# Kernel tuning notes

Measured on AMD Instinct MI355X. Metric: run time of the kernel, lower is better.

The kernel has to match this reference:

```python
import jax, jax.numpy as jnp
import numpy as np

N = 50000   # nodes
E = 500000  # edges
NEG_SLOPE = 0.2


def _edge_softmax(e, dst, n):
    # softmax over edges grouped by destination node (DGL edge_softmax)
    m = jax.ops.segment_max(e, dst, num_segments=n)          # [N,H]
    ex = jnp.exp(e - m[dst])
    s = jax.ops.segment_sum(ex, dst, num_segments=n)
    return ex / s[dst]


def _gat(h, W, al, ar, b, src, dst, heads, d, Wres=None, act=True):
    # DGL GATConv (eval mode, no dropout)
    n = h.shape[0]
    feat = (h @ W).reshape(n, heads, d)                      # [N,H,D]
    el = jnp.sum(feat * al[None], axis=-1)                   # [N,H]
    er = jnp.sum(feat * ar[None], axis=-1)                   # [N,H]
    e = jax.nn.leaky_relu(el[src] + er[dst], NEG_SLOPE)      # [E,H]
    a = _edge_softmax(e, dst, n)                             # [E,H]
    rst = jax.ops.segment_sum(feat[src] * a[..., None], dst, num_segments=n)  # [N,H,D]
    if Wres is not None:
        res = (h @ Wres).reshape(n, heads, d)
    else:
        res = h.reshape(n, heads, d)                         # identity residual (in == heads*d)
    rst = rst + res + b.reshape(1, heads, d)
    if act:
        rst = jax.nn.elu(rst)
    return rst.reshape(n, heads * d)


def _bn(x, g, b, m, v):
    # BatchNorm1d in eval mode
    return (x - m) * g * jax.lax.rsqrt(v + 1e-5) + b


def setup_inputs() -> dict:
    key = jax.random.key(0)
    ks = jax.random.split(key, 40)
    rn = lambda i, s: jax.random.normal(ks[i], s, jnp.float32) * 0.1
    inp = dict(
        node_feats=jax.random.normal(ks[0], (N, 128), jnp.float32),
        edge_feats=jax.random.normal(ks[1], (E, 64), jnp.float32),
        src=jax.random.randint(ks[2], (E,), 0, N, jnp.int32),
        dst=jax.random.randint(ks[3], (E,), 0, N, jnp.int32),
        # GAT layer 0: 128 -> 8 heads x 16
        W0=rn(4, (128, 128)), al0=rn(5, (8, 16)), ar0=rn(6, (8, 16)), b0=rn(7, (128,)),
        g0=1.0 + rn(8, (128,)), bt0=rn(9, (128,)), m0=rn(10, (128,)),
        v0=1.0 + 0.1 * jax.random.uniform(ks[11], (128,), jnp.float32),
        # GAT layer 1: 128 -> 8 heads x 8 (residual projection)
        W1=rn(12, (128, 64)), al1=rn(13, (8, 8)), ar1=rn(14, (8, 8)), b1=rn(15, (64,)),
        Wres1=rn(16, (128, 64)),
        g1=1.0 + rn(17, (64,)), bt1=rn(18, (64,)), m1=rn(19, (64,)),
        v1=1.0 + 0.1 * jax.random.uniform(ks[20], (64,), jnp.float32),
        # GAT layer 2: 64 -> 1 head x 32 (residual projection, no activation)
        W2=rn(21, (64, 32)), al2=rn(22, (1, 32)), ar2=rn(23, (1, 32)), b2=rn(24, (32,)),
        Wres2=rn(25, (64, 32)),
        g2=1.0 + rn(26, (32,)), bt2=rn(27, (32,)), m2=rn(28, (32,)),
        v2=1.0 + 0.1 * jax.random.uniform(ks[29], (32,), jnp.float32),
        # edge projection 64 -> 128
        We=rn(30, (64, 128)), be=rn(31, (128,)),
        # edge classifier: 192 -> 32 -> 16 -> 2
        Wc1=rn(32, (192, 32)), bc1=rn(33, (32,)),
        Wc2=rn(34, (32, 16)), bc2=rn(35, (16,)),
        Wc3=rn(36, (16, 2)), bc3=rn(37, (2,)),
    )
    return inp


def reference(node_feats, edge_feats, src, dst,
              W0, al0, ar0, b0, g0, bt0, m0, v0,
              W1, al1, ar1, b1, Wres1, g1, bt1, m1, v1,
              W2, al2, ar2, b2, Wres2, g2, bt2, m2, v2,
              We, be, Wc1, bc1, Wc2, bc2, Wc3, bc3):
    h = _bn(_gat(node_feats, W0, al0, ar0, b0, src, dst, 8, 16), g0, bt0, m0, v0)
    h = _bn(_gat(h, W1, al1, ar1, b1, src, dst, 8, 8, Wres1), g1, bt1, m1, v1)
    h = _bn(_gat(h, W2, al2, ar2, b2, src, dst, 1, 32, Wres2, act=False), g2, bt2, m2, v2)
    ef = jax.nn.relu(edge_feats @ We + be)                   # [E,128]
    rep = jnp.concatenate([h[src], h[dst], ef], axis=1)      # [E,192]
    z = jax.nn.relu(rep @ Wc1 + bc1)
    z = jax.nn.relu(z @ Wc2 + bc2)
    return z @ Wc3 + bc3                                     # [E,2]
```

## Files before the change

### kernel.cpp

```cpp
#include <hip/hip_runtime.h>
#include <cfloat>
#include <math.h>

#define NEG_SLOPE 0.2f

typedef short short8 __attribute__((ext_vector_type(8)));
typedef float f32x4 __attribute__((ext_vector_type(4)));

__device__ __forceinline__ short f2bf(float x) {
    unsigned u = __float_as_uint(x);
    u += 0x7fffu + ((u >> 16) & 1u);
    return (short)(u >> 16);
}
__device__ __forceinline__ float bf2f(unsigned short s) {
    return __uint_as_float((unsigned)s << 16);
}

__device__ __forceinline__ void lds_fence() {
    __asm__ __volatile__("s_waitcnt lgkmcnt(0)" ::: "memory");
}


__global__ void count_deg_k(const int* __restrict__ dst, int* __restrict__ deg, int E) {
    int i = blockIdx.x * 256 + threadIdx.x;
    if (i < E) atomicAdd(&deg[dst[i]], 1);
}

__global__ void scanA_k(const int* __restrict__ deg, int* __restrict__ csum, int n) {
    int t = blockIdx.x * 256 + threadIdx.x;
    int ch = (n + 4095) >> 12;
    int beg = t * ch, end = min(beg + ch, n);
    int s = 0;
    for (int i = beg; i < end; ++i) s += deg[i];
    csum[t] = s;
}

__global__ void scanB_k(int* __restrict__ csum) {
    __shared__ int part[1024];
    int tid = threadIdx.x;
    int c[4];
    int s = 0;
#pragma unroll
    for (int i = 0; i < 4; ++i) { c[i] = csum[tid * 4 + i]; s += c[i]; }
    part[tid] = s;
    __syncthreads();
    for (int d = 1; d < 1024; d <<= 1) {
        int v = (tid >= d) ? part[tid - d] : 0;
        __syncthreads();
        part[tid] += v;
        __syncthreads();
    }
    int base = (tid > 0) ? part[tid - 1] : 0;
#pragma unroll
    for (int i = 0; i < 4; ++i) { csum[tid * 4 + i] = base; base += c[i]; }
}

__global__ void scanC_k(const int* __restrict__ deg, const int* __restrict__ csum,
                        int* __restrict__ off, int n, int E) {
    int t = blockIdx.x * 256 + threadIdx.x;
    int ch = (n + 4095) >> 12;
    int beg = t * ch, end = min(beg + ch, n);
    int run = csum[t];
    for (int i = beg; i < end; ++i) { off[i] = run; run += deg[i]; }
    if (t == 0) off[n] = E;
}

__global__ void scatter_k(const int* __restrict__ src, const int* __restrict__ dst,
                          const int* __restrict__ off, int* __restrict__ cur,
                          int* __restrict__ srcp, int E) {
    int i = blockIdx.x * 256 + threadIdx.x;
    if (i >= E) return;
    int d = dst[i];
    int p = off[d] + atomicAdd(&cur[d], 1);
    srcp[p] = src[i];
}


struct WSec { const float* src; short* dst; int K, OUT, base; };

__global__ void conv_w_k(const float* W0, const float* W1, const float* Wr1,
                         const float* W2, const float* Wr2, const float* Wc1,
                         const float* We, const float* Wc2,
                         short* W0T, short* W1T, short* Wr1T, short* W2T, short* Wr2T,
                         short* Wc1aT, short* Wc1bT, short* WeT, short* Wc1T, short* Wc2T) {
    int t = blockIdx.x * 256 + threadIdx.x;
    const float* src; short* dst; int K, OUT, base;
    if      (t < 16384) { src = W0;            dst = W0T;   K = 128; OUT = 128; base = 0; }
    else if (t < 24576) { src = W1;            dst = W1T;   K = 128; OUT = 64;  base = 16384; }
    else if (t < 32768) { src = Wr1;           dst = Wr1T;  K = 128; OUT = 64;  base = 24576; }
    else if (t < 34816) { src = W2;            dst = W2T;   K = 64;  OUT = 32;  base = 32768; }
    else if (t < 36864) { src = Wr2;           dst = Wr2T;  K = 64;  OUT = 32;  base = 34816; }
    else if (t < 37888) { src = Wc1;           dst = Wc1aT; K = 32;  OUT = 32;  base = 36864; }
    else if (t < 38912) { src = Wc1 + 1024;    dst = Wc1bT; K = 32;  OUT = 32;  base = 37888; }
    else if (t < 47104) { src = We;            dst = WeT;   K = 64;  OUT = 128; base = 38912; }
    else if (t < 51200) { src = Wc1 + 64 * 32; dst = Wc1T;  K = 128; OUT = 32;  base = 47104; }
    else if (t < 51712) { src = Wc2;           dst = Wc2T;  K = 32;  OUT = 16;  base = 51200; }
    else return;
    int local = t - base;
    int k = local / OUT, n = local % OUT;
    dst[n * K + k] = f2bf(src[k * OUT + n]);
}


template<int K, int NT1, int NT2, bool C1B16, bool AF32>
__global__ __launch_bounds__(256) void gemmM_k(const void* __restrict__ A,
                                               const short* __restrict__ B1T, void* __restrict__ C1,
                                               const short* __restrict__ B2T, float* __restrict__ C2,
                                               int N) {
    int w = threadIdx.x >> 6, lane = threadIdx.x & 63;
    int tile = blockIdx.x * 4 + w;
    int row0 = tile * 16;
    if (row0 >= N) return;
    int m = lane & 15, q = lane >> 4;
    int arow = row0 + m; if (arow >= N) arow = N - 1;

    constexpr int KT = K / 32;
    short8 Af[KT];
    if constexpr (AF32) {
        const float* Ap = (const float*)A + (size_t)arow * K;
#pragma unroll
        for (int kt = 0; kt < KT; ++kt) {
            float4 x = *(const float4*)&Ap[kt * 32 + q * 8];
            float4 y = *(const float4*)&Ap[kt * 32 + q * 8 + 4];
            short8 s;
            s[0] = f2bf(x.x); s[1] = f2bf(x.y); s[2] = f2bf(x.z); s[3] = f2bf(x.w);
            s[4] = f2bf(y.x); s[5] = f2bf(y.y); s[6] = f2bf(y.z); s[7] = f2bf(y.w);
            Af[kt] = s;
        }
    } else {
        const short* Ap = (const short*)A + (size_t)arow * K;
#pragma unroll
        for (int kt = 0; kt < KT; ++kt)
            Af[kt] = *(const short8*)&Ap[kt * 32 + q * 8];
    }

#pragma unroll
    for (int nt = 0; nt < NT1; ++nt) {
        f32x4 acc = {0.f, 0.f, 0.f, 0.f};
#pragma unroll
        for (int kt = 0; kt < KT; ++kt) {
            short8 b = *(const short8*)&B1T[(size_t)(nt * 16 + m) * K + kt * 32 + q * 8];
            acc = __builtin_amdgcn_mfma_f32_16x16x32_bf16(Af[kt], b, acc, 0, 0, 0);
        }
#pragma unroll
        for (int r = 0; r < 4; ++r) {
            int row = row0 + q * 4 + r;
            if (row < N) {
                if constexpr (C1B16)
                    ((short*)C1)[(size_t)row * (NT1 * 16) + nt * 16 + m] = f2bf(acc[r]);
                else
                    ((float*)C1)[(size_t)row * (NT1 * 16) + nt * 16 + m] = acc[r];
            }
        }
    }
    if constexpr (NT2 > 0) {
#pragma unroll
        for (int nt = 0; nt < NT2; ++nt) {
            f32x4 acc = {0.f, 0.f, 0.f, 0.f};
#pragma unroll
            for (int kt = 0; kt < KT; ++kt) {
                short8 b = *(const short8*)&B2T[(size_t)(nt * 16 + m) * K + kt * 32 + q * 8];
                acc = __builtin_amdgcn_mfma_f32_16x16x32_bf16(Af[kt], b, acc, 0, 0, 0);
            }
#pragma unroll
            for (int r = 0; r < 4; ++r) {
                int row = row0 + q * 4 + r;
                if (row < N)
                    C2[(size_t)row * (NT2 * 16) + nt * 16 + m] = acc[r];
            }
        }
    }
}


template<int H, int D>
__global__ void elr_k(const short* __restrict__ featb, const float* __restrict__ al,
                      const float* __restrict__ ar, float* __restrict__ el,
                      float* __restrict__ er, int n) {
    int i = blockIdx.x * 256 + threadIdx.x;
    if (i >= n * H) return;
    int h = i % H;
    const short* f = featb + (size_t)(i / H) * (H * D) + h * D;
    float sl = 0.f, sr = 0.f;
#pragma unroll
    for (int d = 0; d < D; ++d) {
        float v = bf2f((unsigned short)f[d]);
        sl = fmaf(v, al[h * D + d], sl);
        sr = fmaf(v, ar[h * D + d], sr);
    }
    el[i] = sl; er[i] = sr;
}


template<int H, int D, bool ACT>
__global__ __launch_bounds__(256) void gat_node2_k(
    const int* __restrict__ off, const int* __restrict__ srcp,
    const float* __restrict__ el, const float* __restrict__ er,
    const short* __restrict__ featb,
    const float* __restrict__ res, const float* __restrict__ bias,
    const float* __restrict__ bg, const float* __restrict__ bb,
    const float* __restrict__ bm, const float* __restrict__ bv,
    short* __restrict__ houtb, int N) {
    constexpr int HD = H * D;
    constexpr bool PAIR = (HD > 64);
    constexpr int CH = 64 / H;
    int wv_ = threadIdx.x >> 6;
    int lane = threadIdx.x & 63;
    int n = blockIdx.x * 4 + wv_;
    if (n >= N) return;
    int beg = off[n], end = off[n + 1];

    int hh = lane % H;
    int cc = lane / H;
    float ern = er[(size_t)n * H + hh];

    int k0 = PAIR ? 2 * lane : lane;
    int h0 = k0 / D; if (h0 > H - 1) h0 = H - 1;

    float acc0 = 0.f, acc1 = 0.f, svp = 0.f;

    for (int i0 = beg; i0 < end; i0 += CH) {
        int iw = i0 + cc;
        float wv = 0.f;
        int sidx = 0;
        if (iw < end) {
            sidx = srcp[iw];
            float x = el[(size_t)sidx * H + hh] + ern;
            x = x > 0.f ? x : NEG_SLOPE * x;
            wv = __expf(x);
        }
        svp += wv;
        int lim = min(end - i0, CH);
        for (int r = 0; r < lim; ++r) {
            int sl = r * H + h0;
            float w0 = __shfl(wv, sl, 64);
            int s    = __shfl(sidx, sl, 64);
            if constexpr (PAIR) {
                ushort2 uv = *(const ushort2*)&featb[(size_t)s * HD + k0];
                acc0 = fmaf(w0, bf2f(uv.x), acc0);
                acc1 = fmaf(w0, bf2f(uv.y), acc1);
            } else {
                if (lane < HD)
                    acc0 = fmaf(w0, bf2f((unsigned short)featb[(size_t)s * HD + k0]), acc0);
            }
        }
    }
#pragma unroll
    for (int mm = H; mm < 64; mm <<= 1) svp += __shfl_xor(svp, mm, 64);
    bool has_edges = end > beg;
    float inv0 = has_edges ? 1.f / __shfl(svp, h0, 64) : 0.f;

    if constexpr (PAIR) {
        float2 rs = *(const float2*)&res[(size_t)n * HD + k0];
        float2 bi = *(const float2*)&bias[k0];
        float2 gm = *(const float2*)&bm[k0];
        float2 gv = *(const float2*)&bv[k0];
        float2 gg = *(const float2*)&bg[k0];
        float2 gb = *(const float2*)&bb[k0];
        float x0 = acc0 * inv0 + rs.x + bi.x;
        float x1 = acc1 * inv0 + rs.y + bi.y;
        if (ACT) { x0 = x0 > 0.f ? x0 : expm1f(x0); x1 = x1 > 0.f ? x1 : expm1f(x1); }
        float o0 = (x0 - gm.x) * (gg.x * rsqrtf(gv.x + 1e-5f)) + gb.x;
        float o1 = (x1 - gm.y) * (gg.y * rsqrtf(gv.y + 1e-5f)) + gb.y;
        ushort2 hb;
        hb.x = (unsigned short)f2bf(o0);
        hb.y = (unsigned short)f2bf(o1);
        *(ushort2*)&houtb[(size_t)n * HD + k0] = hb;
    } else {
        if (lane < HD) {
            int k = k0;
            float x = acc0 * inv0 + res[(size_t)n * HD + k] + bias[k];
            if (ACT) x = x > 0.f ? x : expm1f(x);
            float o = (x - bm[k]) * (bg[k] * rsqrtf(bv[k] + 1e-5f)) + bb[k];
            houtb[(size_t)n * HD + k] = f2bf(o);
        }
    }
}


__global__ __launch_bounds__(256) void edge_cls_k(
    const float* __restrict__ u1, const float* __restrict__ u2,
    const float* __restrict__ edf,
    const int* __restrict__ src, const int* __restrict__ dst,
    const short* __restrict__ WeTg, const float* __restrict__ be,
    const short* __restrict__ Wc1Tg, const float* __restrict__ bc1,
    const short* __restrict__ Wc2Tg, const float* __restrict__ bc2,
    const float* __restrict__ Wc3, const float* __restrict__ bc3,
    float* __restrict__ out, int E) {
    __shared__ short efA[4][16 * 136];
    __shared__ short z1A[4][16 * 40];
    __shared__ float z2A[4][16 * 20];

    int t = threadIdx.x;
    int w = t >> 6, lane = t & 63;
    int m = lane & 15, q = lane >> 4;
    short* efW = efA[w];
    short* z1W = z1A[w];
    float* z2W = z2A[w];

    int tiles = (E + 15) >> 4;
    int gw = blockIdx.x * 4 + w;
    int W  = gridDim.x * 4;

    float beh[8];
#pragma unroll
    for (int nt = 0; nt < 8; ++nt) beh[nt] = be[nt * 16 + m];
    float bc1h0 = bc1[m], bc1h1 = bc1[16 + m];
    float bc2h = bc2[m];
    float bc30 = bc3[0], bc31 = bc3[1];

    auto ldrow = [&](int tl, float4& a, float4& b, float4& c, float4& d) {
        int em = tl * 16 + m;
        const float* rp = edf + (size_t)(em < E ? em : E - 1) * 64;
        a = *(const float4*)(rp + q * 8);
        b = *(const float4*)(rp + q * 8 + 4);
        c = *(const float4*)(rp + 32 + q * 8);
        d = *(const float4*)(rp + 32 + q * 8 + 4);
    };

    int tile = gw;
    float4 p0 = {0,0,0,0}, p1 = p0, p2 = p0, p3 = p0;
    if (tile < tiles) ldrow(tile, p0, p1, p2, p3);

    for (; tile < tiles; tile += W) {
        float4 c0 = p0, c1 = p1, c2 = p2, c3 = p3;
        int tn = tile + W;
        if (tn < tiles) ldrow(tn, p0, p1, p2, p3);

        int e0w = tile * 16;

        float u1g[2][4], u2g[2][4];
#pragma unroll
        for (int r = 0; r < 4; ++r) {
            int e = e0w + q * 4 + r;
            int ec = e < E ? e : E - 1;
            int s = src[ec], d = dst[ec];
            u1g[0][r] = u1[(size_t)s * 32 + m];
            u1g[1][r] = u1[(size_t)s * 32 + 16 + m];
            u2g[0][r] = u2[(size_t)d * 32 + m];
            u2g[1][r] = u2[(size_t)d * 32 + 16 + m];
        }

        short8 A0, A1;
        A0[0] = f2bf(c0.x); A0[1] = f2bf(c0.y); A0[2] = f2bf(c0.z); A0[3] = f2bf(c0.w);
        A0[4] = f2bf(c1.x); A0[5] = f2bf(c1.y); A0[6] = f2bf(c1.z); A0[7] = f2bf(c1.w);
        A1[0] = f2bf(c2.x); A1[1] = f2bf(c2.y); A1[2] = f2bf(c2.z); A1[3] = f2bf(c2.w);
        A1[4] = f2bf(c3.x); A1[5] = f2bf(c3.y); A1[6] = f2bf(c3.z); A1[7] = f2bf(c3.w);

#pragma unroll
        for (int nt = 0; nt < 8; ++nt) {
            int col = nt * 16 + m;
            float bias = beh[nt];
            f32x4 acc = {bias, bias, bias, bias};
            short8 b0 = *(const short8*)&WeTg[col * 64 + q * 8];
            short8 b1 = *(const short8*)&WeTg[col * 64 + 32 + q * 8];
            acc = __builtin_amdgcn_mfma_f32_16x16x32_bf16(A0, b0, acc, 0, 0, 0);
            acc = __builtin_amdgcn_mfma_f32_16x16x32_bf16(A1, b1, acc, 0, 0, 0);
#pragma unroll
            for (int r = 0; r < 4; ++r)
                efW[(q * 4 + r) * 136 + col] = f2bf(fmaxf(acc[r], 0.f));
        }
        lds_fence();

        short8 Az[4];
#pragma unroll
        for (int kt = 0; kt < 4; ++kt)
            Az[kt] = *(const short8*)&efW[m * 136 + kt * 32 + q * 8];
#pragma unroll
        for (int nt = 0; nt < 2; ++nt) {
            int col = nt * 16 + m;
            float bias = nt ? bc1h1 : bc1h0;
            f32x4 acc = {bias, bias, bias, bias};
#pragma unroll
            for (int kt = 0; kt < 4; ++kt) {
                short8 b = *(const short8*)&Wc1Tg[col * 128 + kt * 32 + q * 8];
                acc = __builtin_amdgcn_mfma_f32_16x16x32_bf16(Az[kt], b, acc, 0, 0, 0);
            }
#pragma unroll
            for (int r = 0; r < 4; ++r) {
                float z = acc[r] + u1g[nt][r] + u2g[nt][r];
                z1W[(q * 4 + r) * 40 + col] = f2bf(fmaxf(z, 0.f));
            }
        }
        lds_fence();

        {
            short8 Az1 = *(const short8*)&z1W[m * 40 + q * 8];
            short8 Bz  = *(const short8*)&Wc2Tg[m * 32 + q * 8];
            f32x4 acc = {bc2h, bc2h, bc2h, bc2h};
            acc = __builtin_amdgcn_mfma_f32_16x16x32_bf16(Az1, Bz, acc, 0, 0, 0);
#pragma unroll
            for (int r = 0; r < 4; ++r)
                z2W[(q * 4 + r) * 20 + m] = fmaxf(acc[r], 0.f);
        }
        lds_fence();

        if (lane < 16) {
            int e = lane;
            int eg = e0w + e;
            if (eg < E) {
                float a0 = bc30, a1 = bc31;
#pragma unroll
                for (int k = 0; k < 16; ++k) {
                    float z = z2W[e * 20 + k];
                    a0 = fmaf(z, Wc3[k * 2], a0);
                    a1 = fmaf(z, Wc3[k * 2 + 1], a1);
                }
                float2 o = {a0, a1};
                *(float2*)&out[(size_t)eg * 2] = o;
            }
        }
        lds_fence();
    }
}


extern "C" void kernel_launch(void* const* d_in, const int* in_sizes, int n_in,
                              void* d_out, int out_size, void* d_ws, size_t ws_size,
                              hipStream_t stream) {
    const float* node_feats = (const float*)d_in[0];
    const float* edge_feats = (const float*)d_in[1];
    const int*   src  = (const int*)d_in[2];
    const int*   dst  = (const int*)d_in[3];
    const float* W0   = (const float*)d_in[4];
    const float* al0  = (const float*)d_in[5];
    const float* ar0  = (const float*)d_in[6];
    const float* b0   = (const float*)d_in[7];
    const float* g0   = (const float*)d_in[8];
    const float* bt0  = (const float*)d_in[9];
    const float* m0   = (const float*)d_in[10];
    const float* v0   = (const float*)d_in[11];
    const float* W1   = (const float*)d_in[12];
    const float* al1  = (const float*)d_in[13];
    const float* ar1  = (const float*)d_in[14];
    const float* b1   = (const float*)d_in[15];
    const float* Wr1  = (const float*)d_in[16];
    const float* g1   = (const float*)d_in[17];
    const float* bt1  = (const float*)d_in[18];
    const float* m1   = (const float*)d_in[19];
    const float* v1   = (const float*)d_in[20];
    const float* W2   = (const float*)d_in[21];
    const float* al2  = (const float*)d_in[22];
    const float* ar2  = (const float*)d_in[23];
    const float* b2   = (const float*)d_in[24];
    const float* Wr2  = (const float*)d_in[25];
    const float* g2   = (const float*)d_in[26];
    const float* bt2  = (const float*)d_in[27];
    const float* v2m  = (const float*)d_in[28];
    const float* v2v  = (const float*)d_in[29];
    const float* We   = (const float*)d_in[30];
    const float* be   = (const float*)d_in[31];
    const float* Wc1  = (const float*)d_in[32];
    const float* bc1  = (const float*)d_in[33];
    const float* Wc2  = (const float*)d_in[34];
    const float* bc2  = (const float*)d_in[35];
    const float* Wc3  = (const float*)d_in[36];
    const float* bc3  = (const float*)d_in[37];
    float* out = (float*)d_out;

    const int N = in_sizes[0] / 128;
    const int E = in_sizes[2];

    char* p = (char*)d_ws;
    auto alloc = [&](size_t bytes) -> void* {
        void* r = (void*)p;
        p += (bytes + 255) & ~(size_t)255;
        return r;
    };
    int*   deg   = (int*)alloc((size_t)N * 4);
    int*   cur   = (int*)alloc((size_t)N * 4);
    int*   off   = (int*)alloc((size_t)(N + 1) * 4);
    int*   srcp  = (int*)alloc((size_t)E * 4);
    int*   csum  = (int*)alloc(4096 * 4);
    short* featb = (short*)alloc((size_t)N * 128 * 2);
    short* h1b   = (short*)alloc((size_t)N * 128 * 2);
    short* h2b   = (short*)alloc((size_t)N * 64 * 2);
    short* h3b   = (short*)alloc((size_t)N * 32 * 2);
    float* resf  = (float*)alloc((size_t)N * 64 * 4);
    float* u1    = (float*)alloc((size_t)N * 32 * 4);
    float* u2    = (float*)alloc((size_t)N * 32 * 4);
    float* el    = (float*)alloc((size_t)N * 8 * 4);
    float* er    = (float*)alloc((size_t)N * 8 * 4);
    short* W0T   = (short*)alloc(128 * 128 * 2);
    short* W1T   = (short*)alloc(64 * 128 * 2);
    short* Wr1T  = (short*)alloc(64 * 128 * 2);
    short* W2T   = (short*)alloc(32 * 64 * 2);
    short* Wr2T  = (short*)alloc(32 * 64 * 2);
    short* Wc1aT = (short*)alloc(32 * 32 * 2);
    short* Wc1bT = (short*)alloc(32 * 32 * 2);
    short* WeTg  = (short*)alloc(128 * 64 * 2);
    short* Wc1Tg = (short*)alloc(32 * 128 * 2);
    short* Wc2Tg = (short*)alloc(16 * 32 * 2);

    hipMemsetAsync(deg, 0, (size_t)N * 4, stream);
    hipMemsetAsync(cur, 0, (size_t)N * 4, stream);

    int eb = (E + 255) / 256;
    count_deg_k<<<eb, 256, 0, stream>>>(dst, deg, E);
    scanA_k<<<16, 256, 0, stream>>>(deg, csum, N);
    scanB_k<<<1, 1024, 0, stream>>>(csum);
    scanC_k<<<16, 256, 0, stream>>>(deg, csum, off, N, E);
    scatter_k<<<eb, 256, 0, stream>>>(src, dst, off, cur, srcp, E);
    conv_w_k<<<202, 256, 0, stream>>>(W0, W1, Wr1, W2, Wr2, Wc1, We, Wc2,
                                      W0T, W1T, Wr1T, W2T, Wr2T,
                                      Wc1aT, Wc1bT, WeTg, Wc1Tg, Wc2Tg);

    int nb4 = (N + 3) / 4;
    int gtb = ((N + 15) / 16 + 3) / 4;

    gemmM_k<128, 8, 0, true, true><<<gtb, 256, 0, stream>>>(node_feats, W0T, featb, nullptr, nullptr, N);
    elr_k<8, 16><<<(N * 8 + 255) / 256, 256, 0, stream>>>(featb, al0, ar0, el, er, N);
    gat_node2_k<8, 16, true><<<nb4, 256, 0, stream>>>(off, srcp, el, er, featb, node_feats,
                                                      b0, g0, bt0, m0, v0, h1b, N);
    gemmM_k<128, 4, 4, true, false><<<gtb, 256, 0, stream>>>(h1b, W1T, featb, Wr1T, resf, N);
    elr_k<8, 8><<<(N * 8 + 255) / 256, 256, 0, stream>>>(featb, al1, ar1, el, er, N);
    gat_node2_k<8, 8, true><<<nb4, 256, 0, stream>>>(off, srcp, el, er, featb, resf,
                                                     b1, g1, bt1, m1, v1, h2b, N);
    gemmM_k<64, 2, 2, true, false><<<gtb, 256, 0, stream>>>(h2b, W2T, featb, Wr2T, resf, N);
    elr_k<1, 32><<<(N + 255) / 256, 256, 0, stream>>>(featb, al2, ar2, el, er, N);
    gat_node2_k<1, 32, false><<<nb4, 256, 0, stream>>>(off, srcp, el, er, featb, resf,
                                                       b2, g2, bt2, v2m, v2v, h3b, N);
    gemmM_k<32, 2, 2, false, false><<<gtb, 256, 0, stream>>>(h3b, Wc1aT, u1, Wc1bT, u2, N);
    edge_cls_k<<<1024, 256, 0, stream>>>(u1, u2, edge_feats, src, dst,
                                         WeTg, be, Wc1Tg, bc1,
                                         Wc2Tg, bc2, Wc3, bc3, out, E);
}
```

Before: 577.6 us.

## Batch neighbor gathers in GAT aggregation, simplify CSR scatter, shuffle-reduce edge classifier

The GAT aggregation kernel now shuffles up to eight edge weights and indices at once and issues all the feature-row loads before the FMAs, so several independent gathers are in flight per wavefront. CSR construction records each edge's atomic rank during degree counting, which removes the second atomic pass and its memset. The edge classifier computes the final 16->2 layer with cross-lane shuffle reductions instead of an LDS round trip, and drops a shared buffer. It also gains a launch-bounds occupancy hint and a grid sized to the tile count. Costs are more registers per thread and an extra E-sized rank array.

```diff
diff --git a/kernel.cpp b/kernel.cpp
--- a/kernel.cpp
+++ b/kernel.cpp
@@ -5,6 +5,7 @@
 #define NEG_SLOPE 0.2f
 
 typedef short short8 __attribute__((ext_vector_type(8)));
+typedef short short4v __attribute__((ext_vector_type(4)));
 typedef float f32x4 __attribute__((ext_vector_type(4)));
 
 __device__ __forceinline__ short f2bf(float x) {
@@ -21,9 +22,10 @@
 }
 
 
-__global__ void count_deg_k(const int* __restrict__ dst, int* __restrict__ deg, int E) {
+__global__ void count_deg_k(const int* __restrict__ dst, int* __restrict__ deg,
+                            int* __restrict__ rank, int E) {
     int i = blockIdx.x * 256 + threadIdx.x;
-    if (i < E) atomicAdd(&deg[dst[i]], 1);
+    if (i < E) rank[i] = atomicAdd(&deg[dst[i]], 1);
 }
 
 __global__ void scanA_k(const int* __restrict__ deg, int* __restrict__ csum, int n) {
@@ -66,17 +68,13 @@
 }
 
 __global__ void scatter_k(const int* __restrict__ src, const int* __restrict__ dst,
-                          const int* __restrict__ off, int* __restrict__ cur,
+                          const int* __restrict__ off, const int* __restrict__ rank,
                           int* __restrict__ srcp, int E) {
     int i = blockIdx.x * 256 + threadIdx.x;
     if (i >= E) return;
-    int d = dst[i];
-    int p = off[d] + atomicAdd(&cur[d], 1);
-    srcp[p] = src[i];
-}
-
-
-struct WSec { const float* src; short* dst; int K, OUT, base; };
+    srcp[off[dst[i]] + rank[i]] = src[i];
+}
+
 
 __global__ void conv_w_k(const float* W0, const float* W1, const float* Wr1,
                          const float* W2, const float* Wr2, const float* Wc1,
@@ -193,7 +191,7 @@
 
 
 template<int H, int D, bool ACT>
-__global__ __launch_bounds__(256) void gat_node2_k(
+__global__ __launch_bounds__(256) void gat_node3_k(
     const int* __restrict__ off, const int* __restrict__ srcp,
     const float* __restrict__ el, const float* __restrict__ er,
     const short* __restrict__ featb,
@@ -204,6 +202,7 @@
     constexpr int HD = H * D;
     constexpr bool PAIR = (HD > 64);
     constexpr int CH = 64 / H;
+    constexpr int SB = (CH < 8) ? CH : 8;
     int wv_ = threadIdx.x >> 6;
     int lane = threadIdx.x & 63;
     int n = blockIdx.x * 4 + wv_;
@@ -231,17 +230,36 @@
         }
         svp += wv;
         int lim = min(end - i0, CH);
-        for (int r = 0; r < lim; ++r) {
-            int sl = r * H + h0;
-            float w0 = __shfl(wv, sl, 64);
-            int s    = __shfl(sidx, sl, 64);
+        for (int rb = 0; rb < lim; rb += SB) {
+            int bs = lim - rb; if (bs > SB) bs = SB;
+            float ws[SB]; int ss[SB];
+#pragma unroll
+            for (int j = 0; j < SB; ++j) {
+                int sl = (rb + j) * H + h0;
+                ws[j] = __shfl(wv, sl, 64);
+                ss[j] = __shfl(sidx, sl, 64);
+            }
             if constexpr (PAIR) {
-                ushort2 uv = *(const ushort2*)&featb[(size_t)s * HD + k0];
-                acc0 = fmaf(w0, bf2f(uv.x), acc0);
-                acc1 = fmaf(w0, bf2f(uv.y), acc1);
+                unsigned rows[SB];
+#pragma unroll
+                for (int j = 0; j < SB; ++j)
+                    if (j < bs) rows[j] = *(const unsigned*)&featb[(size_t)ss[j] * HD + k0];
+#pragma unroll
+                for (int j = 0; j < SB; ++j)
+                    if (j < bs) {
+                        acc0 = fmaf(ws[j], bf2f((unsigned short)(rows[j] & 0xffffu)), acc0);
+                        acc1 = fmaf(ws[j], bf2f((unsigned short)(rows[j] >> 16)), acc1);
+                    }
             } else {
-                if (lane < HD)
-                    acc0 = fmaf(w0, bf2f((unsigned short)featb[(size_t)s * HD + k0]), acc0);
+                unsigned short rows[SB];
+#pragma unroll
+                for (int j = 0; j < SB; ++j)
+                    if (j < bs && lane < HD)
+                        rows[j] = (unsigned short)featb[(size_t)ss[j] * HD + k0];
+#pragma unroll
+                for (int j = 0; j < SB; ++j)
+                    if (j < bs && lane < HD)
+                        acc0 = fmaf(ws[j], bf2f(rows[j]), acc0);
             }
         }
     }
@@ -278,7 +296,7 @@
 }
 
 
-__global__ __launch_bounds__(256) void edge_cls_k(
+__global__ __launch_bounds__(256, 5) void edge_cls_k(
     const float* __restrict__ u1, const float* __restrict__ u2,
     const float* __restrict__ edf,
     const int* __restrict__ src, const int* __restrict__ dst,
@@ -289,24 +307,19 @@
     float* __restrict__ out, int E) {
     __shared__ short efA[4][16 * 136];
     __shared__ short z1A[4][16 * 40];
-    __shared__ float z2A[4][16 * 20];
 
     int t = threadIdx.x;
     int w = t >> 6, lane = t & 63;
     int m = lane & 15, q = lane >> 4;
     short* efW = efA[w];
     short* z1W = z1A[w];
-    float* z2W = z2A[w];
 
     int tiles = (E + 15) >> 4;
     int gw = blockIdx.x * 4 + w;
     int W  = gridDim.x * 4;
 
-    float beh[8];
-#pragma unroll
-    for (int nt = 0; nt < 8; ++nt) beh[nt] = be[nt * 16 + m];
-    float bc1h0 = bc1[m], bc1h1 = bc1[16 + m];
-    float bc2h = bc2[m];
+    float bc2m = bc2[m];
+    float wc30 = Wc3[m * 2], wc31 = Wc3[m * 2 + 1];
     float bc30 = bc3[0], bc31 = bc3[1];
 
     auto ldrow = [&](int tl, float4& a, float4& b, float4& c, float4& d) {
@@ -350,7 +363,7 @@
 #pragma unroll
         for (int nt = 0; nt < 8; ++nt) {
             int col = nt * 16 + m;
-            float bias = beh[nt];
+            float bias = be[col];
             f32x4 acc = {bias, bias, bias, bias};
             short8 b0 = *(const short8*)&WeTg[col * 64 + q * 8];
             short8 b1 = *(const short8*)&WeTg[col * 64 + 32 + q * 8];
@@ -369,7 +382,7 @@
 #pragma unroll
         for (int nt = 0; nt < 2; ++nt) {
             int col = nt * 16 + m;
-            float bias = nt ? bc1h1 : bc1h0;
+            float bias = bc1[col];
             f32x4 acc = {bias, bias, bias, bias};
 #pragma unroll
             for (int kt = 0; kt < 4; ++kt) {
@@ -387,27 +400,32 @@
         {
             short8 Az1 = *(const short8*)&z1W[m * 40 + q * 8];
             short8 Bz  = *(const short8*)&Wc2Tg[m * 32 + q * 8];
-            f32x4 acc = {bc2h, bc2h, bc2h, bc2h};
+            f32x4 acc = {0.f, 0.f, 0.f, 0.f};
             acc = __builtin_amdgcn_mfma_f32_16x16x32_bf16(Az1, Bz, acc, 0, 0, 0);
-#pragma unroll
-            for (int r = 0; r < 4; ++r)
-                z2W[(q * 4 + r) * 20 + m] = fmaxf(acc[r], 0.f);
-        }
-        lds_fence();
-
-        if (lane < 16) {
-            int e = lane;
-            int eg = e0w + e;
-            if (eg < E) {
-                float a0 = bc30, a1 = bc31;
-#pragma unroll
-                for (int k = 0; k < 16; ++k) {
-                    float z = z2W[e * 20 + k];
-                    a0 = fmaf(z, Wc3[k * 2], a0);
-                    a1 = fmaf(z, Wc3[k * 2 + 1], a1);
+            float a0[4], a1[4];
+#pragma unroll
+            for (int r = 0; r < 4; ++r) {
+                float z = fmaxf(acc[r] + bc2m, 0.f);
+                a0[r] = z * wc30;
+                a1[r] = z * wc31;
+            }
+#pragma unroll
+            for (int dd = 1; dd < 16; dd <<= 1) {
+#pragma unroll
+                for (int r = 0; r < 4; ++r) {
+                    a0[r] += __shfl_xor(a0[r], dd, 64);
+                    a1[r] += __shfl_xor(a1[r], dd, 64);
                 }
-                float2 o = {a0, a1};
-                *(float2*)&out[(size_t)eg * 2] = o;
+            }
+            if (m == 0) {
+#pragma unroll
+                for (int r = 0; r < 4; ++r) {
+                    int eg = e0w + q * 4 + r;
+                    if (eg < E) {
+                        float2 o = {a0[r] + bc30, a1[r] + bc31};
+                        *(float2*)&out[(size_t)eg * 2] = o;
+                    }
+                }
             }
         }
         lds_fence();
@@ -468,8 +486,8 @@
         return r;
     };
     int*   deg   = (int*)alloc((size_t)N * 4);
-    int*   cur   = (int*)alloc((size_t)N * 4);
     int*   off   = (int*)alloc((size_t)(N + 1) * 4);
+    int*   rank  = (int*)alloc((size_t)E * 4);
     int*   srcp  = (int*)alloc((size_t)E * 4);
     int*   csum  = (int*)alloc(4096 * 4);
     short* featb = (short*)alloc((size_t)N * 128 * 2);
@@ -493,14 +511,13 @@
     short* Wc2Tg = (short*)alloc(16 * 32 * 2);
 
     hipMemsetAsync(deg, 0, (size_t)N * 4, stream);
-    hipMemsetAsync(cur, 0, (size_t)N * 4, stream);
 
     int eb = (E + 255) / 256;
-    count_deg_k<<<eb, 256, 0, stream>>>(dst, deg, E);
+    count_deg_k<<<eb, 256, 0, stream>>>(dst, deg, rank, E);
     scanA_k<<<16, 256, 0, stream>>>(deg, csum, N);
     scanB_k<<<1, 1024, 0, stream>>>(csum);
     scanC_k<<<16, 256, 0, stream>>>(deg, csum, off, N, E);
-    scatter_k<<<eb, 256, 0, stream>>>(src, dst, off, cur, srcp, E);
+    scatter_k<<<eb, 256, 0, stream>>>(src, dst, off, rank, srcp, E);
     conv_w_k<<<202, 256, 0, stream>>>(W0, W1, Wr1, W2, Wr2, Wc1, We, Wc2,
                                       W0T, W1T, Wr1T, W2T, Wr2T,
                                       Wc1aT, Wc1bT, WeTg, Wc1Tg, Wc2Tg);
@@ -510,18 +527,20 @@
 
     gemmM_k<128, 8, 0, true, true><<<gtb, 256, 0, stream>>>(node_feats, W0T, featb, nullptr, nullptr, N);
     elr_k<8, 16><<<(N * 8 + 255) / 256, 256, 0, stream>>>(featb, al0, ar0, el, er, N);
-    gat_node2_k<8, 16, true><<<nb4, 256, 0, stream>>>(off, srcp, el, er, featb, node_feats,
+    gat_node3_k<8, 16, true><<<nb4, 256, 0, stream>>>(off, srcp, el, er, featb, node_feats,
                                                       b0, g0, bt0, m0, v0, h1b, N);
     gemmM_k<128, 4, 4, true, false><<<gtb, 256, 0, stream>>>(h1b, W1T, featb, Wr1T, resf, N);
     elr_k<8, 8><<<(N * 8 + 255) / 256, 256, 0, stream>>>(featb, al1, ar1, el, er, N);
-    gat_node2_k<8, 8, true><<<nb4, 256, 0, stream>>>(off, srcp, el, er, featb, resf,
+    gat_node3_k<8, 8, true><<<nb4, 256, 0, stream>>>(off, srcp, el, er, featb, resf,
                                                      b1, g1, bt1, m1, v1, h2b, N);
     gemmM_k<64, 2, 2, true, false><<<gtb, 256, 0, stream>>>(h2b, W2T, featb, Wr2T, resf, N);
     elr_k<1, 32><<<(N + 255) / 256, 256, 0, stream>>>(featb, al2, ar2, el, er, N);
-    gat_node2_k<1, 32, false><<<nb4, 256, 0, stream>>>(off, srcp, el, er, featb, resf,
+    gat_node3_k<1, 32, false><<<nb4, 256, 0, stream>>>(off, srcp, el, er, featb, resf,
                                                        b2, g2, bt2, v2m, v2v, h3b, N);
     gemmM_k<32, 2, 2, false, false><<<gtb, 256, 0, stream>>>(h3b, Wc1aT, u1, Wc1bT, u2, N);
-    edge_cls_k<<<1024, 256, 0, stream>>>(u1, u2, edge_feats, src, dst,
-                                         WeTg, be, Wc1Tg, bc1,
-                                         Wc2Tg, bc2, Wc3, bc3, out, E);
-}
+    int tiles = (E + 15) / 16;
+    int blocks = (tiles + 15) / 16;
+    edge_cls_k<<<blocks, 256, 0, stream>>>(u1, u2, edge_feats, src, dst,
+                                           WeTg, be, Wc1Tg, bc1,
+                                           Wc2Tg, bc2, Wc3, bc3, out, E);
+}
```

Result: slower. 682.5 us (+18.2%).
